# Optimization experiments

Measured on AMD Instinct MI355X. Metric: run time of the kernel, lower is better.

The kernel has to match this reference:

```python
import jax, jax.numpy as jnp
import numpy as np

NUM_BOND_TYPE = 6
NUM_BOND_DIRECTION = 3
N_NODES = 20000
N_EDGES = 320000
HIDDEN = 256
OUT = 256
N_MASK = 2000


def setup_inputs() -> dict:
    key = jax.random.key(0)
    ks = jax.random.split(key, 12)
    x = jax.random.normal(ks[0], (N_NODES, HIDDEN), dtype=jnp.float32)
    edge_index = jax.random.randint(ks[1], (2, N_EDGES), 0, N_NODES, dtype=jnp.int64)
    edge_attr = jax.random.randint(ks[2], (N_EDGES, 2), 0, 3, dtype=jnp.int64)
    mask_node_indices = jax.random.randint(ks[3], (N_MASK,), 0, N_NODES, dtype=jnp.int64)
    # parameters (torch Linear convention: y = x @ W.T + b)
    def xavier(k, shape):
        fan_in, fan_out = shape[1], shape[0]
        lim = float(np.sqrt(6.0 / (fan_in + fan_out)))
        return jax.random.uniform(k, shape, jnp.float32, -lim, lim)
    prelu_a = jnp.asarray(0.25, dtype=jnp.float32)  # torch PReLU default
    W_enc = xavier(ks[4], (HIDDEN, HIDDEN))          # enc_to_dec, no bias
    E1 = xavier(ks[5], (NUM_BOND_TYPE, HIDDEN))
    E2 = xavier(ks[6], (NUM_BOND_DIRECTION, HIDDEN))
    W1 = xavier(ks[7], (2 * HIDDEN, HIDDEN))
    b1 = jnp.zeros((2 * HIDDEN,), jnp.float32)
    W2 = xavier(ks[8], (OUT, 2 * HIDDEN))
    b2 = jnp.zeros((OUT,), jnp.float32)
    return {"x": x, "edge_index": edge_index, "edge_attr": edge_attr,
            "mask_node_indices": mask_node_indices, "prelu_a": prelu_a,
            "W_enc": W_enc, "E1": E1, "E2": E2,
            "W1": W1, "b1": b1, "W2": W2, "b2": b2}


def reference(x, edge_index, edge_attr, mask_node_indices, prelu_a,
              W_enc, E1, E2, W1, b1, W2, b2):
    N = x.shape[0]
    # PReLU -> enc_to_dec linear (no bias) -> zero masked rows
    x = jnp.where(x >= 0, x, prelu_a * x)
    x = x @ W_enc.T
    x = x.at[mask_node_indices].set(0.0)
    # add self loops: (i,i) edges with attr (4, 0)
    loop = jnp.arange(N, dtype=edge_index.dtype)
    ei = jnp.concatenate([edge_index, jnp.stack([loop, loop])], axis=1)  # [2, E+N]
    loop_attr = jnp.concatenate(
        [jnp.full((N, 1), 4, edge_attr.dtype), jnp.zeros((N, 1), edge_attr.dtype)], axis=1)
    ea = jnp.concatenate([edge_attr, loop_attr], axis=0)                 # [E+N, 2]
    edge_emb = E1[ea[:, 0]] + E2[ea[:, 1]]                               # [E+N, D]
    src, dst = ei[0], ei[1]                                              # j -> i
    msg = x[src] + edge_emb                                              # [E+N, D]
    aggr = jax.ops.segment_sum(msg, dst, num_segments=N)                 # [N, D]
    # GIN MLP: Linear -> ReLU -> Linear
    h = jax.nn.relu(aggr @ W1.T + b1)
    return h @ W2.T + b2
```

## Files before the change

### kernel.cpp

```cpp
#include <hip/hip_runtime.h>

#define HIDDEN 256
#define CAP 64

typedef _Float16 h4_t __attribute__((ext_vector_type(4)));
typedef _Float16 h8_t __attribute__((ext_vector_type(8)));
typedef float    f4_t __attribute__((ext_vector_type(4)));

typedef const __attribute__((address_space(1))) void* gbl_ptr_t;
typedef __attribute__((address_space(3))) void*       lds_ptr_t;

__device__ inline f4_t cvt4(h4_t h) {
    f4_t o; o.x = (float)h.x; o.y = (float)h.y; o.z = (float)h.z; o.w = (float)h.w;
    return o;
}

__global__ __launch_bounds__(256) void k_prep(
        const float* __restrict__ x, _Float16* __restrict__ xh,
        const float* __restrict__ prelu_a, int M, int Mpad, int nb_x,
        const int* __restrict__ ei, const int* __restrict__ ea, int E,
        int* __restrict__ cnt, int* __restrict__ csr, int nb_fill,
        const float* __restrict__ W_enc, const float* __restrict__ W1,
        const float* __restrict__ W2, _Float16* __restrict__ Whenc,
        _Float16* __restrict__ Wh1, _Float16* __restrict__ Wh2, int nb_w,
        const int* __restrict__ mask, unsigned char* __restrict__ flags, int NM) {
    int b = blockIdx.x;
    int t = threadIdx.x;
    if (b < nb_x) {
        int base = (b * 256 + t) * 4;
        if (base >= Mpad * HIDDEN) return;
        int row = base >> 8;
        h4_t o;
        if (row < M) {
            float pa = *prelu_a;
            f4_t v = *(const f4_t*)(x + base);
            o.x = (_Float16)(v.x >= 0.f ? v.x : pa * v.x);
            o.y = (_Float16)(v.y >= 0.f ? v.y : pa * v.y);
            o.z = (_Float16)(v.z >= 0.f ? v.z : pa * v.z);
            o.w = (_Float16)(v.w >= 0.f ? v.w : pa * v.w);
        } else {
            o = (h4_t)(_Float16)0.f;
        }
        *(h4_t*)(xh + base) = o;
        return;
    }
    b -= nb_x;
    if (b < nb_fill) {
        int e = b * 256 + t;
        if (e >= E) return;
        int src = ei[e];
        int dst = ei[E + e];
        int combo = ea[2 * e] * 3 + ea[2 * e + 1];
        int slot = atomicAdd(&cnt[dst], 1);
        if (slot < CAP) csr[dst * CAP + slot] = src | (combo << 16);
        return;
    }
    b -= nb_fill;
    if (b < nb_w) {
        const int n0 = HIDDEN * HIDDEN, n1 = 2 * HIDDEN * HIDDEN, n2 = HIDDEN * 2 * HIDDEN;
        int base = (b * 256 + t) * 4;
        const float* s; _Float16* d; int off;
        if (base < n0) { s = W_enc; d = Whenc; off = base; }
        else if (base < n0 + n1) { s = W1; d = Wh1; off = base - n0; }
        else if (base < n0 + n1 + n2) { s = W2; d = Wh2; off = base - n0 - n1; }
        else return;
        f4_t v = *(const f4_t*)(s + off);
        h4_t o; o.x = (_Float16)v.x; o.y = (_Float16)v.y;
        o.z = (_Float16)v.z; o.w = (_Float16)v.w;
        *(h4_t*)(d + off) = o;
        return;
    }
    b -= nb_w;
    {
        int i = b * 256 + t;
        if (i < NM) flags[mask[i]] = 1;
    }
}

__global__ __launch_bounds__(256) void k_aggregate(
        const _Float16* __restrict__ xe,
        const float* __restrict__ E1, const float* __restrict__ E2,
        const int* __restrict__ cnt, const int* __restrict__ csr,
        _Float16* __restrict__ aggr, int N, int Mpad) {
    __shared__ __align__(16) _Float16 e12h[18 * HIDDEN];
    int t = threadIdx.x;
    for (int idx = t; idx < 18 * 64; idx += 256) {
        int combo = idx >> 6, c4 = (idx & 63) * 4;
        int a1 = combo / 3, a2 = combo - a1 * 3;
        f4_t v1 = *(const f4_t*)(E1 + a1 * HIDDEN + c4);
        f4_t v2 = *(const f4_t*)(E2 + a2 * HIDDEN + c4);
        h4_t o;
        o.x = (_Float16)(v1.x + v2.x); o.y = (_Float16)(v1.y + v2.y);
        o.z = (_Float16)(v1.z + v2.z); o.w = (_Float16)(v1.w + v2.w);
        *(h4_t*)(e12h + combo * HIDDEN + c4) = o;
    }
    __syncthreads();
    int node = blockIdx.x * 4 + (t >> 6);
    if (node >= Mpad) return;
    int lane = t & 63;
    int c0 = lane * 4;
    if (node >= N) {
        *(h4_t*)(aggr + (size_t)node * HIDDEN + c0) = (h4_t)(_Float16)0.f;
        return;
    }
    int deg = cnt[node];
    if (deg > CAP) deg = CAP;
    const int* lst = csr + (size_t)node * CAP;
    int pv = (lane < deg) ? lst[lane] : 0;

    h4_t hs = *(const h4_t*)(xe + (size_t)node * HIDDEN + c0);
    h4_t se = *(const h4_t*)(e12h + 12 * HIDDEN + c0);
    f4_t acc = cvt4(hs) + cvt4(se);

    int e = 0;
    for (; e + 7 < deg; e += 8) {
        int p[8]; h4_t hv[8], qv[8];
#pragma unroll
        for (int j = 0; j < 8; ++j) p[j] = __shfl(pv, e + j, 64);
#pragma unroll
        for (int j = 0; j < 8; ++j)
            hv[j] = *(const h4_t*)(xe + (size_t)(p[j] & 0xFFFF) * HIDDEN + c0);
#pragma unroll
        for (int j = 0; j < 8; ++j)
            qv[j] = *(const h4_t*)(e12h + (p[j] >> 16) * HIDDEN + c0);
        h4_t s0 = (hv[0] + qv[0]) + (hv[1] + qv[1]);
        h4_t s1 = (hv[2] + qv[2]) + (hv[3] + qv[3]);
        h4_t s2 = (hv[4] + qv[4]) + (hv[5] + qv[5]);
        h4_t s3 = (hv[6] + qv[6]) + (hv[7] + qv[7]);
        acc += cvt4(s0) + cvt4(s1);
        acc += cvt4(s2) + cvt4(s3);
    }
    for (; e < deg; ++e) {
        int p = __shfl(pv, e, 64);
        h4_t h = *(const h4_t*)(xe + (size_t)(p & 0xFFFF) * HIDDEN + c0);
        h4_t q = *(const h4_t*)(e12h + (p >> 16) * HIDDEN + c0);
        acc += cvt4(h + q);
    }
    h4_t o;
    o.x = (_Float16)acc.x; o.y = (_Float16)acc.y;
    o.z = (_Float16)acc.z; o.w = (_Float16)acc.w;
    *(h4_t*)(aggr + (size_t)node * HIDDEN + c0) = o;
}

template <int K, bool RELU, bool HAS_BIAS, bool OUT_F16, bool MASK>
__global__ __launch_bounds__(128) void k_gemm64x128(
        const _Float16* __restrict__ A, const _Float16* __restrict__ B,
        const float* __restrict__ bias, void* __restrict__ Cout,
        const unsigned char* __restrict__ flags, int Mstore, int N) {
    __shared__ __align__(16) _Float16 As[64 * 32];
    __shared__ __align__(16) _Float16 Bs[128 * 32];
    int t = threadIdx.x;
    int w = t >> 6, L = t & 63;
    int wc = w * 64;
    int m0 = blockIdx.y * 64, n0 = blockIdx.x * 128;
    int lr = L & 15, lk = (L >> 4) * 8;

    f4_t acc[4][4] = {};

    auto stage = [&](int k0) {
#pragma unroll
        for (int i = 0; i < 2; ++i) {
            int c = t + 128 * i;
            __builtin_amdgcn_global_load_lds(
                (gbl_ptr_t)(A + (size_t)(m0 + (c >> 2)) * K + k0 + (c & 3) * 8),
                (lds_ptr_t)(As + c * 8), 16, 0, 0);
        }
#pragma unroll
        for (int i = 0; i < 4; ++i) {
            int c = t + 128 * i;
            __builtin_amdgcn_global_load_lds(
                (gbl_ptr_t)(B + (size_t)(n0 + (c >> 2)) * K + k0 + (c & 3) * 8),
                (lds_ptr_t)(Bs + c * 8), 16, 0, 0);
        }
    };

    stage(0);
    constexpr int NS = K / 32;
#pragma unroll
    for (int s = 0; s < NS; ++s) {
        asm volatile("s_waitcnt vmcnt(0)" ::: "memory");
        __syncthreads();
        h8_t af[4], bf[4];
#pragma unroll
        for (int i = 0; i < 4; ++i) af[i] = *(const h8_t*)&As[(i * 16 + lr) * 32 + lk];
#pragma unroll
        for (int j = 0; j < 4; ++j) bf[j] = *(const h8_t*)&Bs[(wc + j * 16 + lr) * 32 + lk];
        asm volatile("s_waitcnt lgkmcnt(0)" ::: "memory");
        __syncthreads();
        if (s + 1 < NS) stage((s + 1) * 32);
#pragma unroll
        for (int i = 0; i < 4; ++i)
#pragma unroll
            for (int j = 0; j < 4; ++j)
                acc[i][j] = __builtin_amdgcn_mfma_f32_16x16x32_f16(af[i], bf[j], acc[i][j], 0, 0, 0);
    }

    int lr4 = (L >> 4) * 4;
#pragma unroll
    for (int i = 0; i < 4; ++i)
#pragma unroll
        for (int r = 0; r < 4; ++r) {
            int row = m0 + i * 16 + lr4 + r;
            float zm = 1.f;
            if constexpr (MASK) zm = flags[row] ? 0.f : 1.f;
#pragma unroll
            for (int j = 0; j < 4; ++j) {
                int col = n0 + wc + j * 16 + lr;
                float v = acc[i][j][r];
                if constexpr (HAS_BIAS) v += bias[col];
                if constexpr (RELU) v = v > 0.f ? v : 0.f;
                v *= zm;
                if constexpr (OUT_F16) {
                    ((_Float16*)Cout)[(size_t)row * N + col] = (_Float16)v;
                } else {
                    if (row < Mstore) ((float*)Cout)[(size_t)row * N + col] = v;
                }
            }
        }
}

extern "C" void kernel_launch(void* const* d_in, const int* in_sizes, int n_in,
                              void* d_out, int out_size, void* d_ws, size_t ws_size,
                              hipStream_t stream) {
    const float* x       = (const float*)d_in[0];
    const int*   ei      = (const int*)d_in[1];
    const int*   ea      = (const int*)d_in[2];
    const int*   mask    = (const int*)d_in[3];
    const float* prelu_a = (const float*)d_in[4];
    const float* W_enc   = (const float*)d_in[5];
    const float* E1      = (const float*)d_in[6];
    const float* E2      = (const float*)d_in[7];
    const float* W1      = (const float*)d_in[8];
    const float* b1      = (const float*)d_in[9];
    const float* W2      = (const float*)d_in[10];
    const float* b2      = (const float*)d_in[11];
    float*       out     = (float*)d_out;

    int N  = in_sizes[0] / HIDDEN;
    int E  = in_sizes[1] / 2;
    int NM = in_sizes[3];
    int Mpad = ((N + 127) / 128) * 128;

    char* ws = (char*)d_ws;
    size_t off = 0;
    _Float16* xh    = (_Float16*)(ws + off); off += (size_t)Mpad * HIDDEN * 2;
    _Float16* XEh   = (_Float16*)(ws + off); off += (size_t)Mpad * HIDDEN * 2;
    _Float16* AGh   = (_Float16*)(ws + off); off += (size_t)Mpad * HIDDEN * 2;
    _Float16* Hh    = (_Float16*)(ws + off); off += (size_t)Mpad * 2 * HIDDEN * 2;
    _Float16* Whenc = (_Float16*)(ws + off); off += (size_t)HIDDEN * HIDDEN * 2;
    _Float16* Wh1   = (_Float16*)(ws + off); off += (size_t)2 * HIDDEN * HIDDEN * 2;
    _Float16* Wh2   = (_Float16*)(ws + off); off += (size_t)HIDDEN * 2 * HIDDEN * 2;
    int* cnt        = (int*)(ws + off);      off += (size_t)N * 4;
    unsigned char* flags = (unsigned char*)(ws + off); off += (size_t)Mpad;
    off = (off + 15) & ~(size_t)15;
    int* csr        = (int*)(ws + off);      off += (size_t)N * CAP * 4;

    hipMemsetAsync(cnt, 0, (size_t)N * 4 + (size_t)Mpad, stream);

    int nb_x    = (Mpad * HIDDEN / 4 + 255) / 256;
    int nb_fill = (E + 255) / 256;
    int wtot4   = (HIDDEN * HIDDEN + 2 * HIDDEN * HIDDEN + HIDDEN * 2 * HIDDEN) / 4;
    int nb_w    = (wtot4 + 255) / 256;
    int nb_m    = (NM + 255) / 256;
    k_prep<<<nb_x + nb_fill + nb_w + nb_m, 256, 0, stream>>>(
        x, xh, prelu_a, N, Mpad, nb_x,
        ei, ea, E, cnt, csr, nb_fill,
        W_enc, W1, W2, Whenc, Wh1, Wh2, nb_w,
        mask, flags, NM);

    dim3 g1(HIDDEN / 128, Mpad / 64);
    k_gemm64x128<HIDDEN, false, false, true, true><<<g1, 128, 0, stream>>>(
        xh, Whenc, nullptr, XEh, flags, N, HIDDEN);

    k_aggregate<<<(Mpad + 3) / 4, 256, 0, stream>>>(XEh, E1, E2, cnt, csr, AGh, N, Mpad);

    dim3 g2(2 * HIDDEN / 128, Mpad / 64);
    k_gemm64x128<HIDDEN, true, true, true, false><<<g2, 128, 0, stream>>>(
        AGh, Wh1, b1, Hh, nullptr, N, 2 * HIDDEN);

    dim3 g3(HIDDEN / 128, Mpad / 64);
    k_gemm64x128<2 * HIDDEN, false, true, false, false><<<g3, 128, 0, stream>>>(
        Hh, Wh2, b2, out, nullptr, N, HIDDEN);
}
```

Before: 179.2 us.

## Fuse PReLU/fp16 conversion into first GEMM and merge CSR fill into it

The first GEMM now loads fp32 x and W_enc directly, applies PReLU and converts to fp16 while staging into LDS. This removes the separate xh and Whenc buffers and their write/read round trip. The CSR edge fill and the W1/W2 conversion run as extra blocks in the same launch, and a small init kernel replaces the memset and writes the mask flags. The trade-offs are register-staged loads with no double buffering and a possibly worse inner GEMM loop.

```diff
diff --git a/kernel.cpp b/kernel.cpp
--- a/kernel.cpp
+++ b/kernel.cpp
@@ -15,66 +15,155 @@
     return o;
 }
 
-__global__ __launch_bounds__(256) void k_prep(
-        const float* __restrict__ x, _Float16* __restrict__ xh,
-        const float* __restrict__ prelu_a, int M, int Mpad, int nb_x,
+__global__ __launch_bounds__(256) void k_init(
+        int* __restrict__ cnt, unsigned char* __restrict__ flags,
+        const int* __restrict__ mask, int N, int Mpad, int NM) {
+    int b = blockIdx.x, t = threadIdx.x;
+    if (b == 0) {
+        unsigned int* f4p = (unsigned int*)flags;
+        for (int i = t; i < Mpad / 4; i += 256) f4p[i] = 0;
+        __syncthreads();
+        for (int i = t; i < NM; i += 256) flags[mask[i]] = 1;
+        return;
+    }
+    int i = (b - 1) * 256 + t;
+    if (i < N) cnt[i] = 0;
+}
+
+__global__ __launch_bounds__(128) void k_gemm1_prep(
+        const float* __restrict__ x, const float* __restrict__ W_enc,
+        const float* __restrict__ prelu_a, _Float16* __restrict__ XEh,
+        const unsigned char* __restrict__ flags,
         const int* __restrict__ ei, const int* __restrict__ ea, int E,
-        int* __restrict__ cnt, int* __restrict__ csr, int nb_fill,
-        const float* __restrict__ W_enc, const float* __restrict__ W1,
-        const float* __restrict__ W2, _Float16* __restrict__ Whenc,
-        _Float16* __restrict__ Wh1, _Float16* __restrict__ Wh2, int nb_w,
-        const int* __restrict__ mask, unsigned char* __restrict__ flags, int NM) {
-    int b = blockIdx.x;
-    int t = threadIdx.x;
-    if (b < nb_x) {
-        int base = (b * 256 + t) * 4;
-        if (base >= Mpad * HIDDEN) return;
-        int row = base >> 8;
-        h4_t o;
-        if (row < M) {
-            float pa = *prelu_a;
-            f4_t v = *(const f4_t*)(x + base);
-            o.x = (_Float16)(v.x >= 0.f ? v.x : pa * v.x);
-            o.y = (_Float16)(v.y >= 0.f ? v.y : pa * v.y);
-            o.z = (_Float16)(v.z >= 0.f ? v.z : pa * v.z);
-            o.w = (_Float16)(v.w >= 0.f ? v.w : pa * v.w);
+        int* __restrict__ cnt, int* __restrict__ csr,
+        const float* __restrict__ W1, const float* __restrict__ W2,
+        _Float16* __restrict__ Wh1, _Float16* __restrict__ Wh2,
+        int N, int NT, int nb_fill) {
+    __shared__ __align__(16) _Float16 As[64 * 32];
+    __shared__ __align__(16) _Float16 Bs[128 * 32];
+    int b = blockIdx.x, t = threadIdx.x;
+
+    if (b >= NT) {
+        int u = b - NT;
+        if (u < nb_fill) {
+            int e = u * 128 + t;
+            if (e < E) {
+                int src = ei[e];
+                int dst = ei[E + e];
+                int combo = ea[2 * e] * 3 + ea[2 * e + 1];
+                int slot = atomicAdd(&cnt[dst], 1);
+                if (slot < CAP) csr[dst * CAP + slot] = src | (combo << 16);
+            }
         } else {
-            o = (h4_t)(_Float16)0.f;
-        }
-        *(h4_t*)(xh + base) = o;
+            const int n1 = 2 * HIDDEN * HIDDEN;
+            int base = ((u - nb_fill) * 128 + t) * 4;
+            const float* s; _Float16* d; int off;
+            if (base < n1) { s = W1; d = Wh1; off = base; }
+            else           { s = W2; d = Wh2; off = base - n1; }
+            f4_t v = *(const f4_t*)(s + off);
+            h4_t o; o.x = (_Float16)v.x; o.y = (_Float16)v.y;
+            o.z = (_Float16)v.z; o.w = (_Float16)v.w;
+            *(h4_t*)(d + off) = o;
+        }
         return;
     }
-    b -= nb_x;
-    if (b < nb_fill) {
-        int e = b * 256 + t;
-        if (e >= E) return;
-        int src = ei[e];
-        int dst = ei[E + e];
-        int combo = ea[2 * e] * 3 + ea[2 * e + 1];
-        int slot = atomicAdd(&cnt[dst], 1);
-        if (slot < CAP) csr[dst * CAP + slot] = src | (combo << 16);
-        return;
-    }
-    b -= nb_fill;
-    if (b < nb_w) {
-        const int n0 = HIDDEN * HIDDEN, n1 = 2 * HIDDEN * HIDDEN, n2 = HIDDEN * 2 * HIDDEN;
-        int base = (b * 256 + t) * 4;
-        const float* s; _Float16* d; int off;
-        if (base < n0) { s = W_enc; d = Whenc; off = base; }
-        else if (base < n0 + n1) { s = W1; d = Wh1; off = base - n0; }
-        else if (base < n0 + n1 + n2) { s = W2; d = Wh2; off = base - n0 - n1; }
-        else return;
-        f4_t v = *(const f4_t*)(s + off);
-        h4_t o; o.x = (_Float16)v.x; o.y = (_Float16)v.y;
-        o.z = (_Float16)v.z; o.w = (_Float16)v.w;
-        *(h4_t*)(d + off) = o;
-        return;
-    }
-    b -= nb_w;
-    {
-        int i = b * 256 + t;
-        if (i < NM) flags[mask[i]] = 1;
-    }
+
+    int w = t >> 6, L = t & 63;
+    int wc = w * 64;
+    int m0 = (b >> 1) * 64, n0 = (b & 1) * 128;
+    int lr = L & 15, lk = (L >> 4) * 8;
+    float pa = *prelu_a;
+
+    f4_t acc[4][4] = {};
+    f4_t fa32[2][2];
+    f4_t fb32[4][2];
+
+    auto LOADG = [&](int k0) {
+#pragma unroll
+        for (int i = 0; i < 2; ++i) {
+            int c = t + 128 * i;
+            int row = m0 + (c >> 2), col = k0 + (c & 3) * 8;
+            if (row < N) {
+                const float* p = x + (size_t)row * HIDDEN + col;
+                fa32[i][0] = *(const f4_t*)p;
+                fa32[i][1] = *(const f4_t*)(p + 4);
+            } else {
+                fa32[i][0] = (f4_t){0.f, 0.f, 0.f, 0.f};
+                fa32[i][1] = (f4_t){0.f, 0.f, 0.f, 0.f};
+            }
+        }
+#pragma unroll
+        for (int i = 0; i < 4; ++i) {
+            int c = t + 128 * i;
+            const float* p = W_enc + (size_t)(n0 + (c >> 2)) * HIDDEN + k0 + (c & 3) * 8;
+            fb32[i][0] = *(const f4_t*)p;
+            fb32[i][1] = *(const f4_t*)(p + 4);
+        }
+    };
+    auto CVTW = [&]() {
+#pragma unroll
+        for (int i = 0; i < 2; ++i) {
+            int c = t + 128 * i;
+            f4_t u = fa32[i][0], v = fa32[i][1];
+            h8_t o;
+            o[0] = (_Float16)(u.x >= 0.f ? u.x : pa * u.x);
+            o[1] = (_Float16)(u.y >= 0.f ? u.y : pa * u.y);
+            o[2] = (_Float16)(u.z >= 0.f ? u.z : pa * u.z);
+            o[3] = (_Float16)(u.w >= 0.f ? u.w : pa * u.w);
+            o[4] = (_Float16)(v.x >= 0.f ? v.x : pa * v.x);
+            o[5] = (_Float16)(v.y >= 0.f ? v.y : pa * v.y);
+            o[6] = (_Float16)(v.z >= 0.f ? v.z : pa * v.z);
+            o[7] = (_Float16)(v.w >= 0.f ? v.w : pa * v.w);
+            *(h8_t*)&As[c * 8] = o;
+        }
+#pragma unroll
+        for (int i = 0; i < 4; ++i) {
+            int c = t + 128 * i;
+            f4_t u = fb32[i][0], v = fb32[i][1];
+            h8_t o;
+            o[0] = (_Float16)u.x; o[1] = (_Float16)u.y;
+            o[2] = (_Float16)u.z; o[3] = (_Float16)u.w;
+            o[4] = (_Float16)v.x; o[5] = (_Float16)v.y;
+            o[6] = (_Float16)v.z; o[7] = (_Float16)v.w;
+            *(h8_t*)&Bs[c * 8] = o;
+        }
+    };
+
+    LOADG(0);
+    constexpr int NS = HIDDEN / 32;
+#pragma unroll
+    for (int s = 0; s < NS; ++s) {
+        CVTW();
+        asm volatile("s_waitcnt lgkmcnt(0)" ::: "memory");
+        __syncthreads();
+        h8_t af[4], bf[4];
+#pragma unroll
+        for (int i = 0; i < 4; ++i) af[i] = *(const h8_t*)&As[(i * 16 + lr) * 32 + lk];
+#pragma unroll
+        for (int j = 0; j < 4; ++j) bf[j] = *(const h8_t*)&Bs[(wc + j * 16 + lr) * 32 + lk];
+        asm volatile("s_waitcnt lgkmcnt(0)" ::: "memory");
+        __syncthreads();
+        if (s + 1 < NS) LOADG((s + 1) * 32);
+#pragma unroll
+        for (int i = 0; i < 4; ++i)
+#pragma unroll
+            for (int j = 0; j < 4; ++j)
+                acc[i][j] = __builtin_amdgcn_mfma_f32_16x16x32_f16(af[i], bf[j], acc[i][j], 0, 0, 0);
+    }
+
+    int lr4 = (L >> 4) * 4;
+#pragma unroll
+    for (int i = 0; i < 4; ++i)
+#pragma unroll
+        for (int r = 0; r < 4; ++r) {
+            int row = m0 + i * 16 + lr4 + r;
+            float zm = flags[row] ? 0.f : 1.f;
+#pragma unroll
+            for (int j = 0; j < 4; ++j) {
+                int col = n0 + wc + j * 16 + lr;
+                XEh[(size_t)row * HIDDEN + col] = (_Float16)(acc[i][j][r] * zm);
+            }
+        }
 }
 
 __global__ __launch_bounds__(256) void k_aggregate(
@@ -243,11 +332,9 @@
 
     char* ws = (char*)d_ws;
     size_t off = 0;
-    _Float16* xh    = (_Float16*)(ws + off); off += (size_t)Mpad * HIDDEN * 2;
     _Float16* XEh   = (_Float16*)(ws + off); off += (size_t)Mpad * HIDDEN * 2;
     _Float16* AGh   = (_Float16*)(ws + off); off += (size_t)Mpad * HIDDEN * 2;
     _Float16* Hh    = (_Float16*)(ws + off); off += (size_t)Mpad * 2 * HIDDEN * 2;
-    _Float16* Whenc = (_Float16*)(ws + off); off += (size_t)HIDDEN * HIDDEN * 2;
     _Float16* Wh1   = (_Float16*)(ws + off); off += (size_t)2 * HIDDEN * HIDDEN * 2;
     _Float16* Wh2   = (_Float16*)(ws + off); off += (size_t)HIDDEN * 2 * HIDDEN * 2;
     int* cnt        = (int*)(ws + off);      off += (size_t)N * 4;
@@ -255,22 +342,15 @@
     off = (off + 15) & ~(size_t)15;
     int* csr        = (int*)(ws + off);      off += (size_t)N * CAP * 4;
 
-    hipMemsetAsync(cnt, 0, (size_t)N * 4 + (size_t)Mpad, stream);
-
-    int nb_x    = (Mpad * HIDDEN / 4 + 255) / 256;
-    int nb_fill = (E + 255) / 256;
-    int wtot4   = (HIDDEN * HIDDEN + 2 * HIDDEN * HIDDEN + HIDDEN * 2 * HIDDEN) / 4;
-    int nb_w    = (wtot4 + 255) / 256;
-    int nb_m    = (NM + 255) / 256;
-    k_prep<<<nb_x + nb_fill + nb_w + nb_m, 256, 0, stream>>>(
-        x, xh, prelu_a, N, Mpad, nb_x,
-        ei, ea, E, cnt, csr, nb_fill,
-        W_enc, W1, W2, Whenc, Wh1, Wh2, nb_w,
-        mask, flags, NM);
-
-    dim3 g1(HIDDEN / 128, Mpad / 64);
-    k_gemm64x128<HIDDEN, false, false, true, true><<<g1, 128, 0, stream>>>(
-        xh, Whenc, nullptr, XEh, flags, N, HIDDEN);
+    k_init<<<1 + (N + 255) / 256, 256, 0, stream>>>(cnt, flags, mask, N, Mpad, NM);
+
+    int NT      = (Mpad / 64) * (HIDDEN / 128);
+    int nb_fill = (E + 127) / 128;
+    int nb_w    = (2 * 2 * HIDDEN * HIDDEN / 4) / 128;
+    k_gemm1_prep<<<NT + nb_fill + nb_w, 128, 0, stream>>>(
+        x, W_enc, prelu_a, XEh, flags,
+        ei, ea, E, cnt, csr, W1, W2, Wh1, Wh2,
+        N, NT, nb_fill);
 
     k_aggregate<<<(Mpad + 3) / 4, 256, 0, stream>>>(XEh, E1, E2, cnt, csr, AGh, N, Mpad);
 
```

Measured after the change: 172.0 us (median of 2 runs). -4.0%, faster.
